# Performance work log

Hardware: AMD Instinct MI355X
Metric: run time of the kernel (lower is better)

The kernel has to match this reference:

```python
import jax, jax.numpy as jnp
import numpy as np

P = 10      # qubits
LQ = 4      # re-uploading layers
B = 4096    # batch
HID = 32    # readout hidden
DIM = 2 ** P


def _rz(t):
    t = jnp.asarray(t, jnp.float32)
    e = jnp.exp(-0.5j * t.astype(jnp.complex64))
    z = jnp.zeros_like(e)
    return jnp.stack([jnp.stack([e, z], -1), jnp.stack([z, jnp.conj(e)], -1)], -2)


def _rx(t):
    t = jnp.asarray(t, jnp.float32)
    c = jnp.cos(0.5 * t).astype(jnp.complex64)
    s = jnp.sin(0.5 * t).astype(jnp.complex64)
    return jnp.stack([jnp.stack([c, -1j * s], -1), jnp.stack([-1j * s, c], -1)], -2)


def _ry(t):
    t = jnp.asarray(t, jnp.float32)
    c = jnp.cos(0.5 * t).astype(jnp.complex64)
    s = jnp.sin(0.5 * t).astype(jnp.complex64)
    return jnp.stack([jnp.stack([c, -s], -1), jnp.stack([s, c], -1)], -2)


def _apply_1q(state, U, k):
    # state [B, 2^P] complex, U [B,2,2]; wire 0 = most-significant bit (PennyLane order)
    b = state.shape[0]
    s = state.reshape(b, 2 ** k, 2, -1)
    s = jnp.einsum('bij,bajc->baic', U, s)
    return s.reshape(b, -1)


def _apply_cnot(state, c, t):
    b = state.shape[0]
    a, d = min(c, t), max(c, t)
    s = state.reshape(b, 2 ** a, 2, 2 ** (d - a - 1), 2, -1)
    if c == a:  # control = smaller wire index (axis 2), target at axis 4
        hi = jnp.flip(s[:, :, 1], axis=3)  # [b,pre,mid,2,post] -> flip target bit
        s = jnp.stack([s[:, :, 0], hi], axis=2)
    else:       # control = larger wire index (axis 4), target at axis 2
        hi = jnp.flip(s[:, :, :, :, 1], axis=2)  # [b,pre,2,mid,post] -> flip target bit
        s = jnp.stack([s[:, :, :, :, 0], hi], axis=4)
    return s.reshape(b, -1)


def _meas_signs(p):
    # rows 0..p-1: Z_k signs; rows p..2p-1: Z_k Z_{(k+1)%p} signs
    idx = np.arange(2 ** p)
    bits = (idx[None, :] >> (p - 1 - np.arange(p)[:, None])) & 1
    z = (1.0 - 2.0 * bits).astype(np.float32)            # [p, 2^p]
    zz = z * np.roll(z, -1, axis=0)                      # [p, 2^p]
    return jnp.asarray(np.concatenate([z, zz], axis=0))  # [2p, 2^p]


MEAS = _meas_signs(P)


def _circuit_feats(theta, rot_weights, enc_scale, enc_bias):
    b = theta.shape[0]
    # Hadamard on every wire of |0...0> -> uniform superposition
    state = jnp.full((b, DIM), 1.0 / np.sqrt(DIM), dtype=jnp.complex64)
    for l in range(LQ):
        for k in range(P):
            t0 = enc_scale[l, k, 0] * theta[:, k] + enc_bias[l, k, 0]
            t1 = enc_scale[l, k, 1] * theta[:, k] + enc_bias[l, k, 1]
            U_enc = jnp.einsum('bij,bjk->bik', _rx(t1), _rz(t0))  # RX(t1) RZ(t0)
            w = rot_weights[l, k]
            # PennyLane Rot(phi,theta,omega) = RZ(omega) RY(theta) RZ(phi)
            U_rot = _rz(w[2]) @ _ry(w[1]) @ _rz(w[0])
            U = jnp.einsum('ij,bjk->bik', U_rot, U_enc)
            state = _apply_1q(state, U, k)
        for k in range(P):
            state = _apply_cnot(state, k, (k + 1) % P)
    probs = jnp.abs(state) ** 2              # [B, 2^P]
    return probs @ MEAS.T                    # [B, 2P] expectation values


def setup_inputs() -> dict:
    key = jax.random.key(0)
    ks = jax.random.split(key, 4)
    theta = jax.random.uniform(ks[0], (B, P), jnp.float32, -np.pi, np.pi)
    rot_weights = 0.02 * jax.random.normal(ks[1], (LQ, P, 3), dtype=jnp.float32)
    enc_scale = jnp.ones((LQ, P, 2), jnp.float32)   # clamp(0.5,1.5) of ones = ones
    enc_bias = jnp.zeros((LQ, P, 2), jnp.float32)
    n_meas = 2 * P
    W1 = jax.random.normal(ks[2], (HID, n_meas), dtype=jnp.float32) / np.sqrt(n_meas)
    b1 = jnp.zeros((HID,), jnp.float32)
    W2 = jax.random.normal(ks[3], (1, HID), dtype=jnp.float32) / np.sqrt(HID)
    b2 = jnp.zeros((1,), jnp.float32)
    return dict(theta=theta, rot_weights=rot_weights, enc_scale=enc_scale,
                enc_bias=enc_bias, W1=W1, b1=b1, W2=W2, b2=b2)


def reference(theta, rot_weights, enc_scale, enc_bias, W1, b1, W2, b2):
    feats = _circuit_feats(theta, rot_weights, enc_scale, enc_bias)
    h = jax.nn.silu(feats @ W1.T + b1)
    return (h @ W2.T + b2)[:, 0]  # [B]
```

## Files before the change

### kernel.cpp

```cpp
#include <hip/hip_runtime.h>
#include <math.h>

#define NQ   10
#define NLAY 4
#define BATCH 4096
#define HID  32
#define NM   20

typedef float    f2  __attribute__((ext_vector_type(2)));
typedef unsigned u2v __attribute__((ext_vector_type(2)));

struct Tables {
    unsigned col[NLAY + 1][NQ];
    unsigned row[NLAY + 1][NQ];
};

constexpr Tables make_tables() {
    Tables t{};
    unsigned col[NQ] = {}, row[NQ] = {};
    for (int k = 0; k < NQ; ++k) { col[k] = 1u << (NQ - 1 - k); row[k] = 1u << (NQ - 1 - k); }
    for (int l = 0; l <= NLAY; ++l) {
        for (int k = 0; k < NQ; ++k) { t.col[l][k] = col[k]; t.row[l][k] = row[k]; }
        for (int k = 0; k < NQ; ++k) {
            int c = k, tg = (k + 1) % NQ;
            col[c] ^= col[tg];
            row[tg] ^= row[c];
        }
    }
    return t;
}

static constexpr Tables TB = make_tables();

struct cpx { float x, y; };
__device__ __forceinline__ cpx cxmul(cpx a, cpx b) {
    return { fmaf(a.x, b.x, -a.y * b.y), fmaf(a.x, b.y, a.y * b.x) };
}

__device__ __forceinline__ f2 mk2(float a, float b) { f2 r; r[0] = a; r[1] = b; return r; }
__device__ __forceinline__ f2 ffma(f2 a, f2 b, f2 c) { return __builtin_elementwise_fma(a, b, c); }

template<int CTRL>
__device__ __forceinline__ float dppf(float x) {
    return __int_as_float(__builtin_amdgcn_update_dpp(
        0, __float_as_int(x), CTRL, 0xF, 0xF, true));
}

template<unsigned M>
__device__ __forceinline__ float dpplo(float x) {
    static_assert(M < 16u, "dpplo handles masks 0..15");
    if constexpr (M == 0u)       return x;
    else if constexpr (M == 1u)  return dppf<0xB1>(x);
    else if constexpr (M == 2u)  return dppf<0x4E>(x);
    else if constexpr (M == 3u)  return dppf<0x1B>(x);
    else if constexpr (M == 7u)  return dppf<0x141>(x);
    else if constexpr (M == 8u)  return dppf<0x128>(x);
    else if constexpr (M == 15u) return dppf<0x140>(x);
    else if constexpr (M == 4u)  return dppf<0x141>(dppf<0x1B>(x));
    else if constexpr (M == 5u)  return dppf<0x141>(dppf<0x4E>(x));
    else if constexpr (M == 6u)  return dppf<0x141>(dppf<0xB1>(x));
    else if constexpr (M == 9u)  return dppf<0x128>(dppf<0xB1>(x));
    else if constexpr (M == 10u) return dppf<0x128>(dppf<0x4E>(x));
    else if constexpr (M == 11u) return dppf<0x128>(dppf<0x1B>(x));
    else if constexpr (M == 12u) return dppf<0x140>(dppf<0x1B>(x));
    else if constexpr (M == 13u) return dppf<0x140>(dppf<0x4E>(x));
    else                         return dppf<0x140>(dppf<0xB1>(x));
}

__device__ __forceinline__ float swap16sel(float x, bool sel16) {
#if __has_builtin(__builtin_amdgcn_permlane16_swap)
    u2v r = __builtin_amdgcn_permlane16_swap(__float_as_uint(x), __float_as_uint(x), false, false);
    return sel16 ? __uint_as_float(r[0]) : __uint_as_float(r[1]);
#else
    (void)sel16; return __shfl_xor(x, 16);
#endif
}
__device__ __forceinline__ float swap32sel(float x, bool sel32) {
#if __has_builtin(__builtin_amdgcn_permlane32_swap)
    u2v r = __builtin_amdgcn_permlane32_swap(__float_as_uint(x), __float_as_uint(x), false, false);
    return sel32 ? __uint_as_float(r[0]) : __uint_as_float(r[1]);
#else
    (void)sel32; return __shfl_xor(x, 32);
#endif
}
__device__ __forceinline__ float redfold16(float x) {
#if __has_builtin(__builtin_amdgcn_permlane16_swap)
    u2v r = __builtin_amdgcn_permlane16_swap(__float_as_uint(x), __float_as_uint(x), false, false);
    return __uint_as_float(r[0]) + __uint_as_float(r[1]);
#else
    return x + __shfl_xor(x, 16);
#endif
}
__device__ __forceinline__ float redfold32(float x) {
#if __has_builtin(__builtin_amdgcn_permlane32_swap)
    u2v r = __builtin_amdgcn_permlane32_swap(__float_as_uint(x), __float_as_uint(x), false, false);
    return __uint_as_float(r[0]) + __uint_as_float(r[1]);
#else
    return x + __shfl_xor(x, 32);
#endif
}

template<unsigned M>
__device__ __forceinline__ float xlane(float x, bool sel16, bool sel32) {
    if constexpr (M == 0u) return x;
    else if constexpr ((M & 48u) == 48u) return __shfl_xor(x, (int)M);
    else {
        float y = dpplo<M & 15u>(x);
        if constexpr ((M & 48u) == 16u)      y = swap16sel(y, sel16);
        else if constexpr ((M & 48u) == 32u) y = swap32sel(y, sel32);
        return y;
    }
}

__device__ __forceinline__ f2 apply_re(f2 ox, f2 oy, f2 px, f2 py,
                                       f2 ar, f2 ai, f2 br, f2 bi) {
    return ffma(ox, ar, ffma(-oy, ai, ffma(px, br, (-py) * bi)));
}
__device__ __forceinline__ f2 apply_im(f2 ox, f2 oy, f2 px, f2 py,
                                       f2 ar, f2 ai, f2 br, f2 bi) {
    return ffma(ox, ai, ffma(oy, ar, ffma(px, bi, py * br)));
}

template<int L, int K>
__device__ __forceinline__ void apply_gate(f2 (&sre)[8], f2 (&sim)[8],
                                           const float4 (*gm)[2], const int lane,
                                           const bool sel16, const bool sel32) {
    constexpr unsigned v  = TB.col[L][K];
    constexpr unsigned m  = TB.row[L][K];
    constexpr unsigned vl = v >> 4;
    constexpr int vj = (int)(v & 15u), vr = vj >> 1, vs = vj & 1;
    constexpr unsigned ml = m >> 4;
    constexpr int mj = (int)(m & 15u), mjr = mj >> 1, mjs = mj & 1;
    constexpr int gi = L * NQ + K;

    int laneP = 0;
    if constexpr (ml != 0) laneP = __popc((unsigned)lane & ml) & 1;
    const float4 A = gm[gi][laneP];
    f2 occ[2], pcc[2];
    occ[0] = mk2(A.x, A.y); pcc[0] = mk2(A.z, A.w);
    if constexpr (mj != 0) {
        const float4 Bq = gm[gi][laneP ^ 1];
        occ[1] = mk2(Bq.x, Bq.y); pcc[1] = mk2(Bq.z, Bq.w);
    } else { occ[1] = occ[0]; pcc[1] = pcc[0]; }

    f2 ocx[2], ocy[2], pcx[2], pcy[2];
    #pragma unroll
    for (int p_ = 0; p_ < 2; ++p_) {
        const f2 a_ = occ[p_], b_ = occ[p_ ^ mjs];
        const f2 c_ = pcc[p_], d_ = pcc[p_ ^ mjs];
        ocx[p_] = mk2(a_[0], b_[0]); ocy[p_] = mk2(a_[1], b_[1]);
        pcx[p_] = mk2(c_[0], d_[0]); pcy[p_] = mk2(c_[1], d_[1]);
    }

    f2 pre[8], pim[8];
    #pragma unroll
    for (int r = 0; r < 8; ++r) {
        const f2 qre = sre[r ^ vr], qim = sim[r ^ vr];
        const float re0 = vs ? qre[1] : qre[0];
        const float re1 = vs ? qre[0] : qre[1];
        const float im0 = vs ? qim[1] : qim[0];
        const float im1 = vs ? qim[0] : qim[1];
        pre[r] = mk2(xlane<vl>(re0, sel16, sel32), xlane<vl>(re1, sel16, sel32));
        pim[r] = mk2(xlane<vl>(im0, sel16, sel32), xlane<vl>(im1, sel16, sel32));
    }
    #pragma unroll
    for (int r = 0; r < 8; ++r) {
        const int p_ = __builtin_popcount((unsigned)(r & mjr)) & 1;
        const f2 nre = apply_re(ocx[p_], ocy[p_], pcx[p_], pcy[p_],
                                sre[r], sim[r], pre[r], pim[r]);
        const f2 nim = apply_im(ocx[p_], ocy[p_], pcx[p_], pcy[p_],
                                sre[r], sim[r], pre[r], pim[r]);
        sre[r] = nre; sim[r] = nim;
    }
}

__global__ __launch_bounds__(256, 4) void qrh_kernel(
    const float* __restrict__ theta, const float* __restrict__ rotw,
    const float* __restrict__ escale, const float* __restrict__ ebias,
    const float* __restrict__ W1, const float* __restrict__ b1,
    const float* __restrict__ W2, const float* __restrict__ b2,
    float* __restrict__ out)
{
    __shared__ float4 gmat[4][NLAY * NQ][2];
    __shared__ float4 wtab[4][NQ];

    const int tid  = threadIdx.x;
    const int lane = tid & 63;
    const int wv   = tid >> 6;
    const int b    = blockIdx.x * 4 + wv;

    bool sel16 = false, sel32 = false;
#if __has_builtin(__builtin_amdgcn_permlane16_swap)
    {
        u2v r = __builtin_amdgcn_permlane16_swap((unsigned)lane, (unsigned)lane, false, false);
        sel16 = (((lane & 16) != 0) == (r[0] == (unsigned)(lane & ~16)));
    }
#endif
#if __has_builtin(__builtin_amdgcn_permlane32_swap)
    {
        u2v r = __builtin_amdgcn_permlane32_swap((unsigned)lane, (unsigned)lane, false, false);
        sel32 = (((lane & 32) != 0) == (r[0] == (unsigned)(lane & ~32)));
    }
#endif

    if (lane < NLAY * NQ) {
        const int g = lane, l = g / NQ, k = g % NQ;
        const float th = theta[b * NQ + k];
        const int e2 = (l * NQ + k) * 2;
        const float t0 = escale[e2 + 0] * th + ebias[e2 + 0];
        const float t1 = escale[e2 + 1] * th + ebias[e2 + 1];
        float sn0, c0, sn1, c1;
        __sincosf(0.5f * t0, &sn0, &c0);
        __sincosf(0.5f * t1, &sn1, &c1);
        const f2 E00 = mk2( c1 * c0,  -c1 * sn0);
        const f2 E01 = mk2( sn1 * sn0, -sn1 * c0);
        const f2 E10 = mk2(-sn1 * sn0, -sn1 * c0);
        const f2 E11 = mk2( c1 * c0,   c1 * sn0);
        const int r3 = (l * NQ + k) * 3;
        const float w0 = rotw[r3 + 0], w1 = rotw[r3 + 1], w2 = rotw[r3 + 2];
        float cw, sw, ca0, sa0, ca1, sa1;
        __sincosf(0.5f * w1, &sw, &cw);
        __sincosf(0.5f * (w0 + w2), &sa0, &ca0);
        __sincosf(0.5f * (w0 - w2), &sa1, &ca1);
        const f2 R00 = mk2( cw * ca0, -cw * sa0);
        const f2 R01 = mk2(-sw * ca1, -sw * sa1);
        const f2 R10 = mk2( sw * ca1, -sw * sa1);
        const f2 R11 = mk2( cw * ca0,  cw * sa0);
        auto cm = [](f2 a, f2 bb) { return mk2(a[0]*bb[0] - a[1]*bb[1], a[0]*bb[1] + a[1]*bb[0]); };
        const f2 U00 = cm(R00, E00) + cm(R01, E10);
        const f2 U01 = cm(R00, E01) + cm(R01, E11);
        const f2 U10 = cm(R10, E00) + cm(R11, E10);
        const f2 U11 = cm(R10, E01) + cm(R11, E11);
        gmat[wv][g][0] = make_float4(U00[0], U00[1], U01[0], U01[1]);
        gmat[wv][g][1] = make_float4(U11[0], U11[1], U10[0], U10[1]);
        if (l == 0) {
            const float inv = 0.70710678118654752f;
            const f2 al = (U00 + U01) * inv;
            const f2 be = (U10 + U11) * inv;
            wtab[wv][k] = make_float4(al[0], al[1], be[0], be[1]);
        }
    }
    __syncthreads();

    f2 sre[8], sim[8];
    {
        cpx pre;
        {
            const float4 q = wtab[wv][0];
            pre = ((lane >> 5) & 1) ? cpx{q.z, q.w} : cpx{q.x, q.y};
            #pragma unroll
            for (int k = 1; k < 6; ++k) {
                const float4 t = wtab[wv][k];
                const cpx w_ = ((lane >> (5 - k)) & 1) ? cpx{t.z, t.w} : cpx{t.x, t.y};
                pre = cxmul(pre, w_);
            }
        }
        const float4 q6 = wtab[wv][6], q7 = wtab[wv][7];
        const float4 q8 = wtab[wv][8], q9 = wtab[wv][9];
        const cpx w6[2] = {{q6.x, q6.y}, {q6.z, q6.w}};
        const cpx w7[2] = {{q7.x, q7.y}, {q7.z, q7.w}};
        const cpx w8[2] = {{q8.x, q8.y}, {q8.z, q8.w}};
        const cpx w9[2] = {{q9.x, q9.y}, {q9.z, q9.w}};
        cpx ph[4], tlo[4];
        #pragma unroll
        for (int a = 0; a < 4; ++a) {
            ph[a]  = cxmul(pre, cxmul(w6[a >> 1], w7[a & 1]));
            tlo[a] = cxmul(w8[a >> 1], w9[a & 1]);
        }
        #pragma unroll
        for (int r = 0; r < 8; ++r) {
            const int j0 = 2 * r, j1 = 2 * r + 1;
            const cpx a0 = cxmul(ph[j0 >> 2], tlo[j0 & 3]);
            const cpx a1 = cxmul(ph[j1 >> 2], tlo[j1 & 3]);
            sre[r] = mk2(a0.x, a1.x);
            sim[r] = mk2(a0.y, a1.y);
        }
    }

    const float4 (*gm)[2] = gmat[wv];

    #define GATE(L,K) apply_gate<L,K>(sre, sim, gm, lane, sel16, sel32);
    #define LAYER(L) GATE(L,0) GATE(L,1) GATE(L,2) GATE(L,3) GATE(L,4) \
                     GATE(L,5) GATE(L,6) GATE(L,7) GATE(L,8) GATE(L,9)
    LAYER(1)
    LAYER(2)
    LAYER(3)
    #undef LAYER
    #undef GATE

    float w[16];
    #pragma unroll
    for (int r = 0; r < 8; ++r) {
        const f2 p2 = ffma(sre[r], sre[r], sim[r] * sim[r]);
        w[2 * r] = p2[0]; w[2 * r + 1] = p2[1];
    }
    #pragma unroll
    for (int bit = 1; bit < 16; bit <<= 1) {
        #pragma unroll
        for (int j = 0; j < 16; ++j) {
            if (!(j & bit)) {
                const float a = w[j], c = w[j | bit];
                w[j] = a + c; w[j | bit] = a - c;
            }
        }
    }

    float feats[NM];
    #pragma unroll
    for (int f = 0; f < NM; ++f) {
        const unsigned M = (f < NQ) ? TB.row[NLAY][f]
                                    : (TB.row[NLAY][f - NQ] ^ TB.row[NLAY][(f - NQ + 1) % NQ]);
        const int Ml = (int)(M >> 4), Mj = (int)(M & 15u);
        const float s = w[Mj];
        const int lsgn = __popc((unsigned)lane & (unsigned)Ml) & 1;
        feats[f] = lsgn ? -s : s;
    }
    #pragma unroll
    for (int f = 0; f < NM; ++f) {
        float v = feats[f];
        v += dppf<0xB1>(v);
        v += dppf<0x4E>(v);
        v += dppf<0x141>(v);
        v += dppf<0x128>(v);
        v = redfold16(v);
        v = redfold32(v);
        feats[f] = v;
    }

    float part = 0.f;
    if (lane < HID) {
        float acc = b1[lane];
        #pragma unroll
        for (int mm = 0; mm < NM; ++mm) acc = fmaf(feats[mm], W1[lane * NM + mm], acc);
        const float sg = 1.f / (1.f + __expf(-acc));
        part = acc * sg * W2[lane];
    }
    part += dppf<0xB1>(part);
    part += dppf<0x4E>(part);
    part += dppf<0x141>(part);
    part += dppf<0x128>(part);
    part = redfold16(part);
    part = redfold32(part);
    if (lane == 0) out[b] = part + b2[0];
}

extern "C" void kernel_launch(void* const* d_in, const int* in_sizes, int n_in,
                              void* d_out, int out_size, void* d_ws, size_t ws_size,
                              hipStream_t stream) {
    (void)in_sizes; (void)n_in; (void)out_size; (void)d_ws; (void)ws_size;
    const float* theta = (const float*)d_in[0];
    const float* rotw  = (const float*)d_in[1];
    const float* esc   = (const float*)d_in[2];
    const float* ebi   = (const float*)d_in[3];
    const float* W1    = (const float*)d_in[4];
    const float* b1    = (const float*)d_in[5];
    const float* W2    = (const float*)d_in[6];
    const float* b2    = (const float*)d_in[7];
    float* out = (float*)d_out;

    qrh_kernel<<<BATCH / 4, 256, 0, stream>>>(theta, rotw, esc, ebi, W1, b1, W2, b2, out);
}
```

Baseline: 102.4 us.

## Store state as interleaved complex pairs and apply gates with packed complex MAC

Switches the per-lane state from split real/imag packed vectors (two amplitudes per f2) to one f2 per amplitude holding (re, im), and rewrites the gate update as two packed complex multiply-accumulates. This drops the pairing and permutation shuffles of gate coefficients and the in-register swaps needed when the partner index differs in the low bit. The cost is swizzle operands (mk2 broadcasts and re/im swaps) on each cmac, and packed FMAs now do one complex amplitude each, so the FMA count per gate may rise.

```diff
diff --git a/kernel.cpp b/kernel.cpp
--- a/kernel.cpp
+++ b/kernel.cpp
@@ -39,6 +39,12 @@
 
 __device__ __forceinline__ f2 mk2(float a, float b) { f2 r; r[0] = a; r[1] = b; return r; }
 __device__ __forceinline__ f2 ffma(f2 a, f2 b, f2 c) { return __builtin_elementwise_fma(a, b, c); }
+
+__device__ __forceinline__ f2 cmac(f2 acc, f2 a, f2 b) {
+    acc = ffma(mk2(a[0], a[0]), b, acc);
+    acc = ffma(mk2(-a[1], a[1]), mk2(b[1], b[0]), acc);
+    return acc;
+}
 
 template<int CTRL>
 __device__ __forceinline__ float dppf(float x) {
@@ -112,65 +118,44 @@
     }
 }
 
-__device__ __forceinline__ f2 apply_re(f2 ox, f2 oy, f2 px, f2 py,
-                                       f2 ar, f2 ai, f2 br, f2 bi) {
-    return ffma(ox, ar, ffma(-oy, ai, ffma(px, br, (-py) * bi)));
-}
-__device__ __forceinline__ f2 apply_im(f2 ox, f2 oy, f2 px, f2 py,
-                                       f2 ar, f2 ai, f2 br, f2 bi) {
-    return ffma(ox, ai, ffma(oy, ar, ffma(px, bi, py * br)));
-}
-
 template<int L, int K>
-__device__ __forceinline__ void apply_gate(f2 (&sre)[8], f2 (&sim)[8],
+__device__ __forceinline__ void apply_gate(f2 (&st)[16],
                                            const float4 (*gm)[2], const int lane,
                                            const bool sel16, const bool sel32) {
     constexpr unsigned v  = TB.col[L][K];
     constexpr unsigned m  = TB.row[L][K];
     constexpr unsigned vl = v >> 4;
-    constexpr int vj = (int)(v & 15u), vr = vj >> 1, vs = vj & 1;
+    constexpr int      vr = (int)(v & 15u);
     constexpr unsigned ml = m >> 4;
-    constexpr int mj = (int)(m & 15u), mjr = mj >> 1, mjs = mj & 1;
-    constexpr int gi = L * NQ + K;
+    constexpr int      mr = (int)(m & 15u);
+    constexpr int      gi = L * NQ + K;
 
     int laneP = 0;
     if constexpr (ml != 0) laneP = __popc((unsigned)lane & ml) & 1;
     const float4 A = gm[gi][laneP];
-    f2 occ[2], pcc[2];
-    occ[0] = mk2(A.x, A.y); pcc[0] = mk2(A.z, A.w);
-    if constexpr (mj != 0) {
-        const float4 Bq = gm[gi][laneP ^ 1];
-        occ[1] = mk2(Bq.x, Bq.y); pcc[1] = mk2(Bq.z, Bq.w);
-    } else { occ[1] = occ[0]; pcc[1] = pcc[0]; }
-
-    f2 ocx[2], ocy[2], pcx[2], pcy[2];
-    #pragma unroll
-    for (int p_ = 0; p_ < 2; ++p_) {
-        const f2 a_ = occ[p_], b_ = occ[p_ ^ mjs];
-        const f2 c_ = pcc[p_], d_ = pcc[p_ ^ mjs];
-        ocx[p_] = mk2(a_[0], b_[0]); ocy[p_] = mk2(a_[1], b_[1]);
-        pcx[p_] = mk2(c_[0], d_[0]); pcy[p_] = mk2(c_[1], d_[1]);
-    }
-
-    f2 pre[8], pim[8];
-    #pragma unroll
-    for (int r = 0; r < 8; ++r) {
-        const f2 qre = sre[r ^ vr], qim = sim[r ^ vr];
-        const float re0 = vs ? qre[1] : qre[0];
-        const float re1 = vs ? qre[0] : qre[1];
-        const float im0 = vs ? qim[1] : qim[0];
-        const float im1 = vs ? qim[0] : qim[1];
-        pre[r] = mk2(xlane<vl>(re0, sel16, sel32), xlane<vl>(re1, sel16, sel32));
-        pim[r] = mk2(xlane<vl>(im0, sel16, sel32), xlane<vl>(im1, sel16, sel32));
-    }
-    #pragma unroll
-    for (int r = 0; r < 8; ++r) {
-        const int p_ = __builtin_popcount((unsigned)(r & mjr)) & 1;
-        const f2 nre = apply_re(ocx[p_], ocy[p_], pcx[p_], pcy[p_],
-                                sre[r], sim[r], pre[r], pim[r]);
-        const f2 nim = apply_im(ocx[p_], ocy[p_], pcx[p_], pcy[p_],
-                                sre[r], sim[r], pre[r], pim[r]);
-        sre[r] = nre; sim[r] = nim;
+    const f2 ocA = mk2(A.x, A.y), pcA = mk2(A.z, A.w);
+    f2 ocB = ocA, pcB = pcA;
+    if constexpr (mr != 0) {
+        const float4 B = gm[gi][laneP ^ 1];
+        ocB = mk2(B.x, B.y); pcB = mk2(B.z, B.w);
+    }
+
+    f2 pv[16];
+    #pragma unroll
+    for (int r = 0; r < 16; ++r) {
+        const f2 q = st[r ^ vr];
+        if constexpr (vl == 0u) pv[r] = q;
+        else pv[r] = mk2(xlane<vl>(q[0], sel16, sel32), xlane<vl>(q[1], sel16, sel32));
+    }
+    #pragma unroll
+    for (int r = 0; r < 16; ++r) {
+        const int pr = __builtin_popcount((unsigned)(r & mr)) & 1;
+        const f2 oc = pr ? ocB : ocA;
+        const f2 pc = pr ? pcB : pcA;
+        f2 acc = mk2(0.f, 0.f);
+        acc = cmac(acc, oc, st[r]);
+        acc = cmac(acc, pc, pv[r]);
+        st[r] = acc;
     }
 }
 
@@ -242,7 +227,7 @@
     }
     __syncthreads();
 
-    f2 sre[8], sim[8];
+    f2 st[16];
     {
         cpx pre;
         {
@@ -268,18 +253,15 @@
             tlo[a] = cxmul(w8[a >> 1], w9[a & 1]);
         }
         #pragma unroll
-        for (int r = 0; r < 8; ++r) {
-            const int j0 = 2 * r, j1 = 2 * r + 1;
-            const cpx a0 = cxmul(ph[j0 >> 2], tlo[j0 & 3]);
-            const cpx a1 = cxmul(ph[j1 >> 2], tlo[j1 & 3]);
-            sre[r] = mk2(a0.x, a1.x);
-            sim[r] = mk2(a0.y, a1.y);
+        for (int r = 0; r < 16; ++r) {
+            const cpx a0 = cxmul(ph[r >> 2], tlo[r & 3]);
+            st[r] = mk2(a0.x, a0.y);
         }
     }
 
     const float4 (*gm)[2] = gmat[wv];
 
-    #define GATE(L,K) apply_gate<L,K>(sre, sim, gm, lane, sel16, sel32);
+    #define GATE(L,K) apply_gate<L,K>(st, gm, lane, sel16, sel32);
     #define LAYER(L) GATE(L,0) GATE(L,1) GATE(L,2) GATE(L,3) GATE(L,4) \
                      GATE(L,5) GATE(L,6) GATE(L,7) GATE(L,8) GATE(L,9)
     LAYER(1)
@@ -290,9 +272,9 @@
 
     float w[16];
     #pragma unroll
-    for (int r = 0; r < 8; ++r) {
-        const f2 p2 = ffma(sre[r], sre[r], sim[r] * sim[r]);
-        w[2 * r] = p2[0]; w[2 * r + 1] = p2[1];
+    for (int r = 0; r < 16; ++r) {
+        const f2 sq = st[r] * st[r];
+        w[r] = sq[0] + sq[1];
     }
     #pragma unroll
     for (int bit = 1; bit < 16; bit <<= 1) {
```

Measured after the change: 100.2 us. 2.1% less time.
